# Performance work log

Measured on AMD Instinct MI355X. Metric: run time of the kernel, lower is better.

The kernel has to match this reference:

```python
import jax, jax.numpy as jnp
import numpy as np

N_PREV = 65536
BATCH = 2048
DIM = 128


def setup_inputs() -> dict:
    key = jax.random.key(0)
    k1, k2 = jax.random.split(key)
    n = N_PREV + BATCH
    target_lib = jax.random.normal(k1, (n, DIM), dtype=jnp.float32)
    reached_lib = jax.random.normal(k2, (n, DIM), dtype=jnp.float32)
    return {
        "target_goal_embedding_library": target_lib,
        "reached_goal_embedding_library": reached_lib,
        "batch_size": BATCH,
    }


def reference(target_goal_embedding_library, reached_goal_embedding_library, batch_size):
    # slice the library: last batch_size rows are current target/reached goals
    tg = target_goal_embedding_library[-batch_size:]      # [B, D]
    rg = reached_goal_embedding_library[-batch_size:]     # [B, D]
    prev = reached_goal_embedding_library[:-batch_size]   # [N_prev, D]

    # brute-force squared euclidean distances via gram trick: [B, N_prev]
    d2 = (
        jnp.sum(tg * tg, axis=-1, keepdims=True)
        - 2.0 * tg @ prev.T
        + jnp.sum(prev * prev, axis=-1)[None, :]
    )
    idx = jnp.argmin(d2, axis=1)          # top-1 nearest neighbor ids, [B]
    closest = prev[idx]                   # [B, D] gather

    # LP(g, s, r) = ||g - s|| - ||g - r||; value and grad wrt g, vmapped over batch
    def LP(g, s, r):
        return (
            jnp.sqrt(jnp.sum(jnp.square(g - s), axis=-1))
            - jnp.sqrt(jnp.sum(jnp.square(g - r), axis=-1))
        )

    IM_vals, IM_grads = jax.vmap(jax.value_and_grad(LP, 0), in_axes=(0, 0, 0))(
        tg, closest, rg
    )
    return IM_vals, IM_grads
```

## Files before the change

kernel.cpp:

```cpp
#include <hip/hip_runtime.h>
#include <math.h>

#define DIM 128
#define BATCH 2048
#define NPREV 65536
#define NCH 64
#define DELTA 0.8f

typedef __attribute__((ext_vector_type(8))) short bf16x8;
typedef __attribute__((ext_vector_type(4))) float f32x4;
typedef unsigned short u16;

static __device__ __forceinline__ unsigned short f2bf(float f) {
    unsigned int u = __float_as_uint(f);
    u += 0x7FFF + ((u >> 16) & 1);
    return (unsigned short)(u >> 16);
}

__global__ __launch_bounds__(256) void k_convB(const float* __restrict__ src,
                                               u16* __restrict__ dst,
                                               float* __restrict__ p2part) {
    int id = blockIdx.x * 256 + threadIdx.x;
    int lane = id & 63, frag = id >> 6;
    int fn = frag & 3, s = (frag >> 2) & 3, jt = (frag >> 4) & 15, chunk = frag >> 8;
    int srow = chunk * 1024 + jt * 64 + fn * 16 + (lane & 15);
    int scol = (s >> 1) * 64 + (s & 1) * 32 + (lane >> 4) * 8;
    const float* sp = src + (size_t)srow * DIM + scol;
    float4 f0 = *reinterpret_cast<const float4*>(sp);
    float4 f1 = *reinterpret_cast<const float4*>(sp + 4);
    float f[8] = {f0.x, f0.y, f0.z, f0.w, f1.x, f1.y, f1.z, f1.w};
    union { unsigned short us[8]; uint4 v; } o;
    float sum = 0.f;
    #pragma unroll
    for (int e = 0; e < 8; ++e) { o.us[e] = f2bf(f[e]); sum += f[e] * f[e]; }
    *reinterpret_cast<uint4*>(dst + (size_t)id * 8) = o.v;
    p2part[srow * 16 + (scol >> 3)] = sum;
}

__global__ __launch_bounds__(256) void k_prev2r(const float* __restrict__ p2part,
                                                float* __restrict__ p2h) {
    int row = blockIdx.x * 256 + threadIdx.x;
    const float4* p = reinterpret_cast<const float4*>(p2part + (size_t)row * 16);
    float4 a = p[0], b = p[1], c = p[2], d = p[3];
    float s = ((a.x + a.y) + (a.z + a.w)) + ((b.x + b.y) + (b.z + b.w))
            + ((c.x + c.y) + (c.z + c.w)) + ((d.x + d.y) + (d.z + d.w));
    p2h[row] = -0.5f * s;
}

__global__ __launch_bounds__(256) void k_convA(const float* __restrict__ src,
                                               u16* __restrict__ dst) {
    int id = blockIdx.x * 256 + threadIdx.x;
    int lane = id & 63, frag = id >> 6;
    int fm = frag & 3, s = (frag >> 2) & 3, strip = frag >> 4;
    int srow = strip * 64 + fm * 16 + (lane & 15);
    int scol = (s >> 1) * 64 + (s & 1) * 32 + (lane >> 4) * 8;
    const float* sp = src + (size_t)srow * DIM + scol;
    float4 f0 = *reinterpret_cast<const float4*>(sp);
    float4 f1 = *reinterpret_cast<const float4*>(sp + 4);
    float f[8] = {f0.x, f0.y, f0.z, f0.w, f1.x, f1.y, f1.z, f1.w};
    union { unsigned short us[8]; uint4 v; } o;
    #pragma unroll
    for (int e = 0; e < 8; ++e) o.us[e] = f2bf(f[e]);
    *reinterpret_cast<uint4*>(dst + (size_t)id * 8) = o.v;
}

__global__ __launch_bounds__(256, 2) void k_gemm_argmin(
    const u16* __restrict__ Aimg, const u16* __restrict__ Bimg,
    const float* __restrict__ p2h, float4* __restrict__ partial)
{
    const int t = threadIdx.x;
    const int lane = t & 63;
    const int w = t >> 6;
    const int l15 = lane & 15;
    const int lhi = lane >> 4;

    const int bid = blockIdx.x;
    const int chunk = bid & 63;
    const int strip = (bid >> 6) * 4 + w;

    bf16x8 areg[4][4];
    {
        const u16* ab = Aimg + ((size_t)strip * 16) * 512 + (size_t)lane * 8;
        #pragma unroll
        for (int s = 0; s < 4; ++s)
            #pragma unroll
            for (int fm = 0; fm < 4; ++fm)
                areg[s][fm] = *reinterpret_cast<const bf16x8*>(ab + (s * 4 + fm) * 512);
    }

    const u16* gb = Bimg + ((size_t)chunk * 256) * 512 + (size_t)lane * 8;
    const int phbase = chunk * 1024 + l15;
    const f32x4 z4 = {0.f, 0.f, 0.f, 0.f};

    float v1[4][4], v2[4][4];
    #pragma unroll
    for (int fm = 0; fm < 4; ++fm)
        #pragma unroll
        for (int r = 0; r < 4; ++r) { v1[fm][r] = -INFINITY; v2[fm][r] = -INFINITY; }

    f32x4 acc[4][4];
    bf16x8 bk0[4], bk1[4];

    #pragma unroll
    for (int fn = 0; fn < 4; ++fn)
        bk0[fn] = *reinterpret_cast<const bf16x8*>(gb + fn * 512);

#define LOADBANK(BK, G) { \
        const u16* gp_ = gb + (size_t)(G) * 2048; \
        BK[0] = *reinterpret_cast<const bf16x8*>(gp_); \
        BK[1] = *reinterpret_cast<const bf16x8*>(gp_ + 512); \
        BK[2] = *reinterpret_cast<const bf16x8*>(gp_ + 1024); \
        BK[3] = *reinterpret_cast<const bf16x8*>(gp_ + 1536); }

#define MFMA_STAGE_INIT(BK, S) \
        _Pragma("unroll") \
        for (int fm = 0; fm < 4; ++fm) \
            _Pragma("unroll") \
            for (int fn = 0; fn < 4; ++fn) \
                acc[fm][fn] = __builtin_amdgcn_mfma_f32_16x16x32_bf16(areg[S][fm], BK[fn], z4, 0, 0, 0);

#define MFMA_STAGE_ACC(BK, S) \
        _Pragma("unroll") \
        for (int fm = 0; fm < 4; ++fm) \
            _Pragma("unroll") \
            for (int fn = 0; fn < 4; ++fn) \
                acc[fm][fn] = __builtin_amdgcn_mfma_f32_16x16x32_bf16(areg[S][fm], BK[fn], acc[fm][fn], 0, 0, 0);

    for (int jt = 0; jt < 16; ++jt) {
        const int g0 = jt * 4;
        float ph[4];
        #pragma unroll
        for (int fn = 0; fn < 4; ++fn) ph[fn] = p2h[phbase + jt * 64 + fn * 16];

        LOADBANK(bk1, g0 + 1);
        __builtin_amdgcn_s_setprio(1);
        MFMA_STAGE_INIT(bk0, 0);
        __builtin_amdgcn_s_setprio(0);
        LOADBANK(bk0, g0 + 2);
        __builtin_amdgcn_s_setprio(1);
        MFMA_STAGE_ACC(bk1, 1);
        __builtin_amdgcn_s_setprio(0);
        LOADBANK(bk1, g0 + 3);
        __builtin_amdgcn_s_setprio(1);
        MFMA_STAGE_ACC(bk0, 2);
        __builtin_amdgcn_s_setprio(0);
        if (jt + 1 < 16) LOADBANK(bk0, g0 + 4);
        __builtin_amdgcn_s_setprio(1);
        MFMA_STAGE_ACC(bk1, 3);
        __builtin_amdgcn_s_setprio(0);

        const unsigned stamp = (unsigned)l15 | ((unsigned)jt << 4);
        #pragma unroll
        for (int fm = 0; fm < 4; ++fm) {
            #pragma unroll
            for (int r = 0; r < 4; ++r) {
                float s0 = acc[fm][0][r] + ph[0];
                float s1 = acc[fm][1][r] + ph[1];
                float s2 = acc[fm][2][r] + ph[2];
                float s3 = acc[fm][3][r] + ph[3];
                float m = fmaxf(fmaxf(s0, s1), fmaxf(s2, s3));
                float key = __uint_as_float((__float_as_uint(m) & ~0x7FFu) | stamp);
                float tm = fminf(v1[fm][r], key);
                v1[fm][r] = fmaxf(v1[fm][r], key);
                v2[fm][r] = fmaxf(v2[fm][r], tm);
            }
        }
    }
#undef LOADBANK
#undef MFMA_STAGE_INIT
#undef MFMA_STAGE_ACC

    #pragma unroll
    for (int fm = 0; fm < 4; ++fm) {
        #pragma unroll
        for (int r = 0; r < 4; ++r) {
            float a1 = v1[fm][r], a2 = v2[fm][r];
            #pragma unroll
            for (int m = 1; m < 16; m <<= 1) {
                float o1 = __shfl_xor(a1, m), o2 = __shfl_xor(a2, m);
                float n2 = fmaxf(fminf(a1, o1), fmaxf(a2, o2));
                a1 = fmaxf(a1, o1); a2 = n2;
            }
            if (l15 == 0) {
                unsigned ua = __float_as_uint(a1), ub = __float_as_uint(a2);
                int row = strip * 64 + fm * 16 + lhi * 4 + r;
                int ja = chunk * 1024 + (int)((ua >> 4) & 15) * 64 + (int)(ua & 15);
                int jb = chunk * 1024 + (int)((ub >> 4) & 15) * 64 + (int)(ub & 15);
                partial[(size_t)row * NCH + chunk] = make_float4(
                    -2.0f * __uint_as_float(ua & ~0x7FFu), __int_as_float(ja),
                    -2.0f * __uint_as_float(ub & ~0x7FFu), __int_as_float(jb));
            }
        }
    }
}

__global__ __launch_bounds__(256) void k_final2(
    const float* __restrict__ tg, const float* __restrict__ rg,
    const float* __restrict__ prev, const float4* __restrict__ partial,
    float* __restrict__ out_vals, float* __restrict__ out_grads)
{
    const int wv = threadIdx.x >> 6, lane = threadIdx.x & 63;
    const int i = blockIdx.x * 4 + wv;
    const float4 e = partial[(size_t)i * NCH + lane];

    float bv = e.x;
    #pragma unroll
    for (int m = 1; m < 64; m <<= 1) bv = fminf(bv, __shfl_xor(bv, m));

    unsigned long long m1 = __ballot(e.x <= bv + DELTA);
    unsigned long long m2 = __ballot(e.z <= bv + DELTA);
    const float2 g = *reinterpret_cast<const float2*>(tg + (size_t)i * DIM + 2 * lane);
    const int j1i = __float_as_int(e.y), j2i = __float_as_int(e.w);

    float bestd = INFINITY; int bestj = 0x7fffffff;
    while (m1 | m2) {
        int j0;
        if (m1) { int src = __ffsll(m1) - 1; m1 &= m1 - 1; j0 = __shfl(j1i, src); }
        else    { int src = __ffsll(m2) - 1; m2 &= m2 - 1; j0 = __shfl(j2i, src); }
        #pragma unroll
        for (int f = 0; f < 4; ++f) {
            int cj = j0 + f * 16;
            const float2 p = *reinterpret_cast<const float2*>(prev + (size_t)cj * DIM + 2 * lane);
            float dx = g.x - p.x, dy = g.y - p.y;
            float d = dx * dx + dy * dy;
            #pragma unroll
            for (int m = 1; m < 64; m <<= 1) d += __shfl_xor(d, m);
            if (d < bestd || (d == bestd && cj < bestj)) { bestd = d; bestj = cj; }
        }
    }

    const float2 s = *reinterpret_cast<const float2*>(prev + (size_t)bestj * DIM + 2 * lane);
    const float2 r = *reinterpret_cast<const float2*>(rg + (size_t)i * DIM + 2 * lane);
    const float dsx = g.x - s.x, dsy = g.y - s.y;
    const float drx = g.x - r.x, dry = g.y - r.y;
    float ds = dsx * dsx + dsy * dsy;
    float dr = drx * drx + dry * dry;
    #pragma unroll
    for (int m = 1; m < 64; m <<= 1) { ds += __shfl_xor(ds, m); dr += __shfl_xor(dr, m); }
    const float sds = sqrtf(ds), sdr = sqrtf(dr);
    if (lane == 0) out_vals[i] = sds - sdr;
    const float is = 1.0f / sds, ir = 1.0f / sdr;
    float2 gr;
    gr.x = dsx * is - drx * ir;
    gr.y = dsy * is - dry * ir;
    *reinterpret_cast<float2*>(out_grads + (size_t)i * DIM + 2 * lane) = gr;
}

#define TM 128
#define TN 128
#define FNCHUNK 16
#define JT_PER_CHUNK 32

__global__ __launch_bounds__(256) void k_prev2(const float* __restrict__ prev,
                                               float* __restrict__ prev2,
                                               int nprev) {
    const int wave = threadIdx.x >> 6;
    const int lane = threadIdx.x & 63;
    const int row = blockIdx.x * 4 + wave;
    if (row >= nprev) return;
    const float2 v = *reinterpret_cast<const float2*>(prev + (size_t)row * DIM + 2 * lane);
    float s = v.x * v.x + v.y * v.y;
    #pragma unroll
    for (int m = 1; m < 64; m <<= 1) s += __shfl_xor(s, m);
    if (lane == 0) prev2[row] = s;
}

__global__ __launch_bounds__(256, 1) void k_argmin_fb(
    const float* __restrict__ tg, const float* __restrict__ prev,
    const float* __restrict__ prev2, float2* __restrict__ partial)
{
    __shared__ float4 tgL[TM * 32];
    __shared__ float4 pvL[TN * 32];
    __shared__ float  p2L[TN];
    const int t = threadIdx.x;
    const int rowTile = blockIdx.x;
    const int chunk = blockIdx.y;
    const float4* tgG = reinterpret_cast<const float4*>(tg + (size_t)rowTile * TM * DIM);
    #pragma unroll
    for (int i = 0; i < 16; ++i) {
        const int idx = t + 256 * i;
        const int row = idx >> 5, kk = idx & 31;
        tgL[row * 32 + (kk ^ (row & 7))] = tgG[idx];
    }
    const int tx = t & 15, ty = t >> 4;
    const int sa = ty & 7, sb = tx & 7;
    float minval[8]; int minidx[8];
    #pragma unroll
    for (int ri = 0; ri < 8; ++ri) { minval[ri] = INFINITY; minidx[ri] = 0x7fffffff; }
    const int jchunk0 = chunk * (JT_PER_CHUNK * TN);
    for (int jt = 0; jt < JT_PER_CHUNK; ++jt) {
        const int j0 = jchunk0 + jt * TN;
        __syncthreads();
        const float4* pvG = reinterpret_cast<const float4*>(prev + (size_t)j0 * DIM);
        #pragma unroll
        for (int i = 0; i < 16; ++i) {
            const int idx = t + 256 * i;
            const int row = idx >> 5, kk = idx & 31;
            pvL[row * 32 + (kk ^ (row & 7))] = pvG[idx];
        }
        if (t < TN) p2L[t] = prev2[j0 + t];
        __syncthreads();
        float acc[8][8];
        #pragma unroll
        for (int ri = 0; ri < 8; ++ri)
            #pragma unroll
            for (int ci = 0; ci < 8; ++ci) acc[ri][ci] = 0.f;
        #pragma unroll 2
        for (int kk = 0; kk < 32; ++kk) {
            float4 a[8], b[8];
            const int ka = kk ^ sa, kb = kk ^ sb;
            #pragma unroll
            for (int ri = 0; ri < 8; ++ri) a[ri] = tgL[(ty + 16 * ri) * 32 + ka];
            #pragma unroll
            for (int ci = 0; ci < 8; ++ci) b[ci] = pvL[(tx + 16 * ci) * 32 + kb];
            #pragma unroll
            for (int ri = 0; ri < 8; ++ri)
                #pragma unroll
                for (int ci = 0; ci < 8; ++ci) {
                    acc[ri][ci] += a[ri].x * b[ci].x;
                    acc[ri][ci] += a[ri].y * b[ci].y;
                    acc[ri][ci] += a[ri].z * b[ci].z;
                    acc[ri][ci] += a[ri].w * b[ci].w;
                }
        }
        #pragma unroll
        for (int ci = 0; ci < 8; ++ci) {
            const int jl = tx + 16 * ci;
            const int jg = j0 + jl;
            const float pj = p2L[jl];
            #pragma unroll
            for (int ri = 0; ri < 8; ++ri) {
                const float d = pj - 2.f * acc[ri][ci];
                if (d < minval[ri]) { minval[ri] = d; minidx[ri] = jg; }
            }
        }
    }
    __syncthreads();
    float2* red = reinterpret_cast<float2*>(pvL);
    #pragma unroll
    for (int ri = 0; ri < 8; ++ri) {
        const int row = ty + 16 * ri;
        red[row * 16 + tx] = make_float2(minval[ri], __int_as_float(minidx[ri]));
    }
    __syncthreads();
    if (t < TM) {
        float bv = INFINITY; int bi = 0x7fffffff;
        #pragma unroll
        for (int e = 0; e < 16; ++e) {
            const float2 p = red[t * 16 + e];
            const int pi = __float_as_int(p.y);
            if (p.x < bv || (p.x == bv && pi < bi)) { bv = p.x; bi = pi; }
        }
        partial[(size_t)(rowTile * TM + t) * FNCHUNK + chunk] =
            make_float2(bv, __int_as_float(bi));
    }
}

__global__ __launch_bounds__(256) void k_final_fb(
    const float* __restrict__ tg, const float* __restrict__ rg,
    const float* __restrict__ prev, const float2* __restrict__ partial,
    float* __restrict__ out_vals, float* __restrict__ out_grads)
{
    const int wave = threadIdx.x >> 6, lane = threadIdx.x & 63;
    const int i = blockIdx.x * 4 + wave;
    float bv = INFINITY; int bi = 0x7fffffff;
    if (lane < FNCHUNK) {
        const float2 p = partial[(size_t)i * FNCHUNK + lane];
        bv = p.x; bi = __float_as_int(p.y);
    }
    #pragma unroll
    for (int m = 1; m < 16; m <<= 1) {
        const float ov = __shfl_xor(bv, m);
        const int   oi = __shfl_xor(bi, m);
        if (ov < bv || (ov == bv && oi < bi)) { bv = ov; bi = oi; }
    }
    bi = __shfl(bi, 0);
    const float2 g = *reinterpret_cast<const float2*>(tg   + (size_t)i  * DIM + 2 * lane);
    const float2 s = *reinterpret_cast<const float2*>(prev + (size_t)bi * DIM + 2 * lane);
    const float2 r = *reinterpret_cast<const float2*>(rg   + (size_t)i  * DIM + 2 * lane);
    const float dsx = g.x - s.x, dsy = g.y - s.y;
    const float drx = g.x - r.x, dry = g.y - r.y;
    float ds = dsx * dsx + dsy * dsy;
    float dr = drx * drx + dry * dry;
    #pragma unroll
    for (int m = 1; m < 64; m <<= 1) { ds += __shfl_xor(ds, m); dr += __shfl_xor(dr, m); }
    const float sds = sqrtf(ds), sdr = sqrtf(dr);
    if (lane == 0) out_vals[i] = sds - sdr;
    const float is = 1.0f / sds, ir = 1.0f / sdr;
    float2 gr;
    gr.x = dsx * is - drx * ir;
    gr.y = dsy * is - dry * ir;
    *reinterpret_cast<float2*>(out_grads + (size_t)i * DIM + 2 * lane) = gr;
}

extern "C" void kernel_launch(void* const* d_in, const int* in_sizes, int n_in,
                              void* d_out, int out_size, void* d_ws, size_t ws_size,
                              hipStream_t stream) {
    const float* target  = (const float*)d_in[0];
    const float* reached = (const float*)d_in[1];
    const int n_total = in_sizes[0] / DIM;
    const int nprev = n_total - BATCH;

    const float* tg   = target  + (size_t)nprev * DIM;
    const float* rg   = reached + (size_t)nprev * DIM;
    const float* prev = reached;

    float* out_vals  = (float*)d_out;
    float* out_grads = out_vals + BATCH;

    const size_t offB  = 0;
    const size_t offA  = (size_t)16384 * 512 * 2;
    const size_t offP2 = offA + (size_t)512 * 512 * 2;
    const size_t offPP = offP2 + (size_t)NPREV * 4;
    const size_t offPt = offPP + (size_t)NPREV * 16 * 4;
    const size_t need  = offPt + (size_t)BATCH * NCH * sizeof(float4);

    if (nprev == NPREV && ws_size >= need) {
        u16*    Bb      = (u16*)((char*)d_ws + offB);
        u16*    Ab      = (u16*)((char*)d_ws + offA);
        float*  p2h     = (float*)((char*)d_ws + offP2);
        float*  p2part  = (float*)((char*)d_ws + offPP);
        float4* partial = (float4*)((char*)d_ws + offPt);

        k_convB<<<4096, 256, 0, stream>>>(prev, Bb, p2part);
        k_convA<<<128, 256, 0, stream>>>(tg, Ab);
        k_prev2r<<<NPREV / 256, 256, 0, stream>>>(p2part, p2h);
        k_gemm_argmin<<<512, 256, 0, stream>>>(Ab, Bb, p2h, partial);
        k_final2<<<BATCH / 4, 256, 0, stream>>>(tg, rg, prev, partial,
                                                out_vals, out_grads);
    } else {
        float*  prev2   = (float*)d_ws;
        float2* partial = (float2*)((char*)d_ws + (size_t)nprev * sizeof(float));
        k_prev2<<<nprev / 4, 256, 0, stream>>>(prev, prev2, nprev);
        dim3 grid(BATCH / TM, FNCHUNK);
        k_argmin_fb<<<grid, 256, 0, stream>>>(tg, prev, prev2, partial);
        k_final_fb<<<BATCH / 4, 256, 0, stream>>>(tg, rg, prev, partial, out_vals, out_grads);
    }
}
```

Baseline: 64.68 us.

## Split prev library into 128 chunks and shuffle-reduce row norm partials

Halves the GEMM-argmin chunk size from 1024 to 512 columns, doubling the grid to 1024 blocks and the number of per-row partial candidates to 128, which the final kernel now scans with two float4 loads and four ballot masks. Separately, the B conversion kernel reduces squared-norm partials across lanes with shuffles, so only 4 partials per row are written instead of 16, shrinking the p2part buffer and the reduction kernel's reads. The aim is better occupancy and load balance on the many CUs of the GPU. In exchange, each block amortises its A-register load over less work, and the final kernel must read and scan twice as many partials, which can yield more near-tie candidates to verify.

Measured after the change: 66.30 us. 2.5% more time.

```diff
diff --git a/kernel.cpp b/kernel.cpp
--- a/kernel.cpp
+++ b/kernel.cpp
@@ -4,7 +4,8 @@
 #define DIM 128
 #define BATCH 2048
 #define NPREV 65536
-#define NCH 64
+#define NCH 128
+#define NJT 8
 #define DELTA 0.8f
 
 typedef __attribute__((ext_vector_type(8))) short bf16x8;
@@ -22,8 +23,8 @@
                                                float* __restrict__ p2part) {
     int id = blockIdx.x * 256 + threadIdx.x;
     int lane = id & 63, frag = id >> 6;
-    int fn = frag & 3, s = (frag >> 2) & 3, jt = (frag >> 4) & 15, chunk = frag >> 8;
-    int srow = chunk * 1024 + jt * 64 + fn * 16 + (lane & 15);
+    int fn = frag & 3, s = (frag >> 2) & 3, jt = (frag >> 4) & 7, chunk = frag >> 7;
+    int srow = chunk * 512 + jt * 64 + fn * 16 + (lane & 15);
     int scol = (s >> 1) * 64 + (s & 1) * 32 + (lane >> 4) * 8;
     const float* sp = src + (size_t)srow * DIM + scol;
     float4 f0 = *reinterpret_cast<const float4*>(sp);
@@ -34,17 +35,16 @@
     #pragma unroll
     for (int e = 0; e < 8; ++e) { o.us[e] = f2bf(f[e]); sum += f[e] * f[e]; }
     *reinterpret_cast<uint4*>(dst + (size_t)id * 8) = o.v;
-    p2part[srow * 16 + (scol >> 3)] = sum;
+    sum += __shfl_xor(sum, 16);
+    sum += __shfl_xor(sum, 32);
+    if ((lane >> 4) == 0) p2part[srow * 4 + s] = sum;
 }
 
 __global__ __launch_bounds__(256) void k_prev2r(const float* __restrict__ p2part,
                                                 float* __restrict__ p2h) {
     int row = blockIdx.x * 256 + threadIdx.x;
-    const float4* p = reinterpret_cast<const float4*>(p2part + (size_t)row * 16);
-    float4 a = p[0], b = p[1], c = p[2], d = p[3];
-    float s = ((a.x + a.y) + (a.z + a.w)) + ((b.x + b.y) + (b.z + b.w))
-            + ((c.x + c.y) + (c.z + c.w)) + ((d.x + d.y) + (d.z + d.w));
-    p2h[row] = -0.5f * s;
+    const float4 a = *reinterpret_cast<const float4*>(p2part + (size_t)row * 4);
+    p2h[row] = -0.5f * ((a.x + a.y) + (a.z + a.w));
 }
 
 __global__ __launch_bounds__(256) void k_convA(const float* __restrict__ src,
@@ -75,8 +75,8 @@
     const int lhi = lane >> 4;
 
     const int bid = blockIdx.x;
-    const int chunk = bid & 63;
-    const int strip = (bid >> 6) * 4 + w;
+    const int chunk = bid & 127;
+    const int strip = (bid >> 7) * 4 + w;
 
     bf16x8 areg[4][4];
     {
@@ -88,8 +88,8 @@
                 areg[s][fm] = *reinterpret_cast<const bf16x8*>(ab + (s * 4 + fm) * 512);
     }
 
-    const u16* gb = Bimg + ((size_t)chunk * 256) * 512 + (size_t)lane * 8;
-    const int phbase = chunk * 1024 + l15;
+    const u16* gb = Bimg + (size_t)chunk * 65536 + (size_t)lane * 8;
+    const int phbase = chunk * 512 + l15;
     const f32x4 z4 = {0.f, 0.f, 0.f, 0.f};
 
     float v1[4][4], v2[4][4];
@@ -126,7 +126,7 @@
             for (int fn = 0; fn < 4; ++fn) \
                 acc[fm][fn] = __builtin_amdgcn_mfma_f32_16x16x32_bf16(areg[S][fm], BK[fn], acc[fm][fn], 0, 0, 0);
 
-    for (int jt = 0; jt < 16; ++jt) {
+    for (int jt = 0; jt < NJT; ++jt) {
         const int g0 = jt * 4;
         float ph[4];
         #pragma unroll
@@ -144,7 +144,7 @@
         __builtin_amdgcn_s_setprio(1);
         MFMA_STAGE_ACC(bk0, 2);
         __builtin_amdgcn_s_setprio(0);
-        if (jt + 1 < 16) LOADBANK(bk0, g0 + 4);
+        if (jt + 1 < NJT) LOADBANK(bk0, g0 + 4);
         __builtin_amdgcn_s_setprio(1);
         MFMA_STAGE_ACC(bk1, 3);
         __builtin_amdgcn_s_setprio(0);
@@ -184,8 +184,8 @@
             if (l15 == 0) {
                 unsigned ua = __float_as_uint(a1), ub = __float_as_uint(a2);
                 int row = strip * 64 + fm * 16 + lhi * 4 + r;
-                int ja = chunk * 1024 + (int)((ua >> 4) & 15) * 64 + (int)(ua & 15);
-                int jb = chunk * 1024 + (int)((ub >> 4) & 15) * 64 + (int)(ub & 15);
+                int ja = chunk * 512 + (int)((ua >> 4) & 7) * 64 + (int)(ua & 15);
+                int jb = chunk * 512 + (int)((ub >> 4) & 7) * 64 + (int)(ub & 15);
                 partial[(size_t)row * NCH + chunk] = make_float4(
                     -2.0f * __uint_as_float(ua & ~0x7FFu), __int_as_float(ja),
                     -2.0f * __uint_as_float(ub & ~0x7FFu), __int_as_float(jb));
@@ -201,22 +201,28 @@
 {
     const int wv = threadIdx.x >> 6, lane = threadIdx.x & 63;
     const int i = blockIdx.x * 4 + wv;
-    const float4 e = partial[(size_t)i * NCH + lane];
-
-    float bv = e.x;
+    const float4 e0 = partial[(size_t)i * NCH + lane];
+    const float4 e1 = partial[(size_t)i * NCH + 64 + lane];
+
+    float bv = fminf(e0.x, e1.x);
     #pragma unroll
     for (int m = 1; m < 64; m <<= 1) bv = fminf(bv, __shfl_xor(bv, m));
 
-    unsigned long long m1 = __ballot(e.x <= bv + DELTA);
-    unsigned long long m2 = __ballot(e.z <= bv + DELTA);
+    unsigned long long m00 = __ballot(e0.x <= bv + DELTA);
+    unsigned long long m01 = __ballot(e0.z <= bv + DELTA);
+    unsigned long long m10 = __ballot(e1.x <= bv + DELTA);
+    unsigned long long m11 = __ballot(e1.z <= bv + DELTA);
     const float2 g = *reinterpret_cast<const float2*>(tg + (size_t)i * DIM + 2 * lane);
-    const int j1i = __float_as_int(e.y), j2i = __float_as_int(e.w);
+    const int j00 = __float_as_int(e0.y), j01 = __float_as_int(e0.w);
+    const int j10 = __float_as_int(e1.y), j11 = __float_as_int(e1.w);
 
     float bestd = INFINITY; int bestj = 0x7fffffff;
-    while (m1 | m2) {
+    while (m00 | m01 | m10 | m11) {
         int j0;
-        if (m1) { int src = __ffsll(m1) - 1; m1 &= m1 - 1; j0 = __shfl(j1i, src); }
-        else    { int src = __ffsll(m2) - 1; m2 &= m2 - 1; j0 = __shfl(j2i, src); }
+        if (m00)      { int s = __ffsll(m00) - 1; m00 &= m00 - 1; j0 = __shfl(j00, s); }
+        else if (m01) { int s = __ffsll(m01) - 1; m01 &= m01 - 1; j0 = __shfl(j01, s); }
+        else if (m10) { int s = __ffsll(m10) - 1; m10 &= m10 - 1; j0 = __shfl(j10, s); }
+        else          { int s = __ffsll(m11) - 1; m11 &= m11 - 1; j0 = __shfl(j11, s); }
         #pragma unroll
         for (int f = 0; f < 4; ++f) {
             int cj = j0 + f * 16;
@@ -412,7 +418,7 @@
     const size_t offA  = (size_t)16384 * 512 * 2;
     const size_t offP2 = offA + (size_t)512 * 512 * 2;
     const size_t offPP = offP2 + (size_t)NPREV * 4;
-    const size_t offPt = offPP + (size_t)NPREV * 16 * 4;
+    const size_t offPt = offPP + (size_t)NPREV * 4 * 4;
     const size_t need  = offPt + (size_t)BATCH * NCH * sizeof(float4);
 
     if (nprev == NPREV && ws_size >= need) {
@@ -425,7 +431,7 @@
         k_convB<<<4096, 256, 0, stream>>>(prev, Bb, p2part);
         k_convA<<<128, 256, 0, stream>>>(tg, Ab);
         k_prev2r<<<NPREV / 256, 256, 0, stream>>>(p2part, p2h);
-        k_gemm_argmin<<<512, 256, 0, stream>>>(Ab, Bb, p2h, partial);
+        k_gemm_argmin<<<1024, 256, 0, stream>>>(Ab, Bb, p2h, partial);
         k_final2<<<BATCH / 4, 256, 0, stream>>>(tg, rg, prev, partial,
                                                 out_vals, out_grads);
     } else {
```
